# Performance work log

Measured on AMD Instinct MI355X. Metric: run time of the kernel, lower is better.

## Reference

```python
import jax, jax.numpy as jnp
import numpy as np

C = 64          # num_channels
DEPTH = 9       # dilation_depth
REPEAT = 2      # dilation_repeat
K = 2           # kernel_size
DILATIONS = [2 ** j for _ in range(REPEAT) for j in range(DEPTH)]
L = len(DILATIONS)  # 18 gated layers


def causal_conv(x, w, b, dilation):
    # x: [B, Cin, T], w: [Cout, Cin, K] -> [B, Cout, T] with causal (left) padding
    pad = (w.shape[-1] - 1) * dilation
    y = jax.lax.conv_general_dilated(
        x, w, window_strides=(1,), padding=[(pad, 0)],
        rhs_dilation=(dilation,), dimension_numbers=("NCH", "OIH", "NCH"))
    return y + b[None, :, None]


def setup_inputs() -> dict:
    key = jax.random.key(0)
    ks = jax.random.split(key, 9)
    s = 0.1
    x = jax.random.normal(ks[0], (4, 1, 65536), dtype=jnp.float32)
    in_w = jax.random.normal(ks[1], (C, 1, 1), dtype=jnp.float32) * s
    in_b = jax.random.normal(ks[2], (C,), dtype=jnp.float32) * s
    hid_w = jax.random.normal(ks[3], (L, 2 * C, C, K), dtype=jnp.float32) * s
    hid_b = jax.random.normal(ks[4], (L, 2 * C), dtype=jnp.float32) * s
    res_w = jax.random.normal(ks[5], (L, C, C, 1), dtype=jnp.float32) * s
    res_b = jax.random.normal(ks[6], (L, C), dtype=jnp.float32) * s
    mix_w = jax.random.normal(ks[7], (1, C * L, 1), dtype=jnp.float32) * s
    mix_b = jax.random.normal(ks[8], (1,), dtype=jnp.float32) * s
    return {"x": x, "in_w": in_w, "in_b": in_b, "hid_w": hid_w, "hid_b": hid_b,
            "res_w": res_w, "res_b": res_b, "mix_w": mix_w, "mix_b": mix_b}


def reference(x, in_w, in_b, hid_w, hid_b, res_w, res_b, mix_w, mix_b):
    # Input 1x1 conv: [B,1,T] -> [B,C,T]
    out = causal_conv(x, in_w, in_b, 1)
    skips = []
    for i, d in enumerate(DILATIONS):
        xi = out
        h = causal_conv(xi, hid_w[i], hid_b[i], d)       # [B, 2C, T]
        gated = jnp.tanh(h[:, :C]) * jax.nn.sigmoid(h[:, C:])  # [B, C, T]
        skips.append(gated)
        out = causal_conv(gated, res_w[i], res_b[i], 1) + xi    # residual
    skip = jnp.concatenate(skips, axis=1)                # [B, C*L, T]
    return causal_conv(skip, mix_w, mix_b, 1)            # [B, 1, T]
```

## Files before the change

kernel.cpp:

```cpp
#include <hip/hip_runtime.h>
#include <hip/hip_bf16.h>
#include <math.h>

#define NCH 64
#define T_LEN 65536
#define NLAYER 18

typedef __attribute__((ext_vector_type(8))) short bf16x8;
typedef __attribute__((ext_vector_type(4))) short bf16x4;
typedef __attribute__((ext_vector_type(4))) float f32x4;

static __device__ __forceinline__ float bf2f(short s) {
    union { short u[2]; float f; } v;
    v.u[0] = 0; v.u[1] = s;
    return v.f;
}

__global__ void input_conv_kernel(const float* __restrict__ x,
                                  const float* __restrict__ in_w,
                                  const float* __restrict__ in_b,
                                  __hip_bfloat16* __restrict__ out) {
    int gid = blockIdx.x * 256 + threadIdx.x;
    int c8 = gid & 7;
    int t  = (gid >> 3) & (T_LEN - 1);
    int b  = gid >> 19;
    float xv = x[(size_t)b * T_LEN + t];
    bf16x8 v;
#pragma unroll
    for (int j = 0; j < 8; ++j) {
        float o = in_w[c8 * 8 + j] * xv + in_b[c8 * 8 + j];
        __hip_bfloat16 h = __float2bfloat16(o);
        v[j] = *(short*)&h;
    }
    *(bf16x8*)(out + ((size_t)b * T_LEN + t) * NCH + c8 * 8) = v;
}

__global__ void convert_weights_kernel(const float* __restrict__ hid_w,
                                       const float* __restrict__ res_w,
                                       __hip_bfloat16* __restrict__ whid,
                                       __hip_bfloat16* __restrict__ wres) {
    int gid = blockIdx.x * 256 + threadIdx.x;
    if (gid < NLAYER * 128 * 128) {
        int l   = gid >> 14;
        int rem = gid & 16383;
        int o   = rem >> 7;
        int k   = rem & 127;
        float v = (k < 64)
            ? hid_w[((l * 128 + o) * 64 + k) * 2]
            : hid_w[((l * 128 + o) * 64 + (k - 64)) * 2 + 1];
        whid[gid] = __float2bfloat16(v);
    }
    if (gid < NLAYER * 64 * 64) {
        wres[gid] = __float2bfloat16(res_w[gid]);
    }
}

__global__ __launch_bounds__(256, 2) void layer_mfma_kernel(
    const __hip_bfloat16* __restrict__ prev,
    __hip_bfloat16* __restrict__ next,
    float* __restrict__ acc,
    const __hip_bfloat16* __restrict__ whid,
    const float* __restrict__ hb,
    const __hip_bfloat16* __restrict__ wres,
    const float* __restrict__ rb,
    const float* __restrict__ mw,
    int d) {
    __shared__ __align__(16) __hip_bfloat16 Xp[64 * 72];
    __shared__ __align__(16) __hip_bfloat16 Xc[64 * 72];
    __shared__ __align__(16) __hip_bfloat16 Gt[64 * 72];

    const int t0   = blockIdx.x << 6;
    const int tid  = threadIdx.x;
    const int lane = tid & 63;
    const int w4   = tid >> 6;
    const int l15  = lane & 15;
    const int quad = lane >> 4;
    const int m0   = w4 * 16;

    const int rr = tid >> 3;
    const int co = (tid & 7) * 8;

    bf16x8 aT[4], aS[4], aR[2];
    {
        const __hip_bfloat16* whT = whid + (size_t)(m0 + l15) * 128 + quad * 8;
        const __hip_bfloat16* whS = whT + 64 * 128;
#pragma unroll
        for (int k = 0; k < 4; ++k) {
            aT[k] = *(const bf16x8*)(whT + k * 32);
            aS[k] = *(const bf16x8*)(whS + k * 32);
        }
        const __hip_bfloat16* wrA = wres + (size_t)(m0 + l15) * 64 + quad * 8;
        aR[0] = *(const bf16x8*)(wrA);
        aR[1] = *(const bf16x8*)(wrA + 32);
    }
    f32x4 biasT, biasS, biasR;
#pragma unroll
    for (int r = 0; r < 4; ++r) {
        biasT[r] = hb[m0 + quad * 4 + r];
        biasS[r] = hb[64 + m0 + quad * 4 + r];
        biasR[r] = rb[m0 + quad * 4 + r];
    }
    float mwq[16];
#pragma unroll
    for (int j = 0; j < 16; ++j) mwq[j] = mw[quad * 16 + j];

    bf16x8 pc[2], pp[2];
#define LOAD_TILE(b)                                                          \
    do {                                                                      \
        const __hip_bfloat16* pb = prev + ((size_t)(b) * T_LEN + t0) * NCH;   \
        _Pragma("unroll")                                                     \
        for (int pass = 0; pass < 2; ++pass) {                                \
            int r = pass * 32 + rr;                                           \
            pc[pass] = *(const bf16x8*)(pb + r * NCH + co);                   \
            int tp = t0 + r - d;                                              \
            bf16x8 z = {0, 0, 0, 0, 0, 0, 0, 0};                              \
            pp[pass] = z;                                                     \
            if (tp >= 0)                                                      \
                pp[pass] = *(const bf16x8*)(prev +                            \
                    ((size_t)(b) * T_LEN + tp) * NCH + co);                   \
        }                                                                     \
    } while (0)

    LOAD_TILE(0);

#pragma unroll
    for (int b = 0; b < 4; ++b) {
#pragma unroll
        for (int pass = 0; pass < 2; ++pass) {
            int r = pass * 32 + rr;
            *(bf16x8*)(&Xc[r * 72 + co]) = pc[pass];
            *(bf16x8*)(&Xp[r * 72 + co]) = pp[pass];
        }
        __syncthreads();

        if (b < 3) LOAD_TILE(b + 1);

        f32x4 accT[4], accS[4];
#pragma unroll
        for (int nt = 0; nt < 4; ++nt) { accT[nt] = biasT; accS[nt] = biasS; }
#pragma unroll
        for (int ks = 0; ks < 4; ++ks) {
            const __hip_bfloat16* src = (ks < 2) ? Xp : Xc;
            const int kk = (ks & 1) * 32 + quad * 8;
#pragma unroll
            for (int nt = 0; nt < 4; ++nt) {
                bf16x8 bx = *(const bf16x8*)(&src[(nt * 16 + l15) * 72 + kk]);
                accT[nt] = __builtin_amdgcn_mfma_f32_16x16x32_bf16(aT[ks], bx, accT[nt], 0, 0, 0);
                accS[nt] = __builtin_amdgcn_mfma_f32_16x16x32_bf16(aS[ks], bx, accS[nt], 0, 0, 0);
            }
        }

#pragma unroll
        for (int nt = 0; nt < 4; ++nt) {
            int t = nt * 16 + l15;
#pragma unroll
            for (int r = 0; r < 4; ++r) {
                float e2 = __expf(2.f * accT[nt][r]);
                float th = 1.f - 2.f * __builtin_amdgcn_rcpf(e2 + 1.f);
                float sg = __builtin_amdgcn_rcpf(1.f + __expf(-accS[nt][r]));
                Gt[t * 72 + m0 + quad * 4 + r] = __float2bfloat16(th * sg);
            }
        }

        bf16x4 curres[4];
#pragma unroll
        for (int nt = 0; nt < 4; ++nt) {
            curres[nt] = *(const bf16x4*)(&Xc[(nt * 16 + l15) * 72 + m0 + quad * 4]);
        }
        __syncthreads();

        f32x4 accR[4];
#pragma unroll
        for (int nt = 0; nt < 4; ++nt) accR[nt] = biasR;
#pragma unroll
        for (int ks = 0; ks < 2; ++ks) {
            const int kk = ks * 32 + quad * 8;
#pragma unroll
            for (int nt = 0; nt < 4; ++nt) {
                bf16x8 bx = *(const bf16x8*)(&Gt[(nt * 16 + l15) * 72 + kk]);
                accR[nt] = __builtin_amdgcn_mfma_f32_16x16x32_bf16(aR[ks], bx, accR[nt], 0, 0, 0);
            }
        }

        __hip_bfloat16* nb = next + ((size_t)b * T_LEN + t0) * NCH;
#pragma unroll
        for (int nt = 0; nt < 4; ++nt) {
            int t = nt * 16 + l15;
            bf16x4 ov;
#pragma unroll
            for (int r = 0; r < 4; ++r) {
                __hip_bfloat16 h = __float2bfloat16(accR[nt][r] + bf2f(curres[nt][r]));
                ov[r] = *(short*)&h;
            }
            *(bf16x4*)(nb + t * NCH + m0 + quad * 4) = ov;
        }

        {
            int t = w4 * 16 + l15;
            bf16x8 g0 = *(const bf16x8*)(&Gt[t * 72 + quad * 16]);
            bf16x8 g1 = *(const bf16x8*)(&Gt[t * 72 + quad * 16 + 8]);
            float s = 0.f;
#pragma unroll
            for (int j = 0; j < 8; ++j) {
                s += mwq[j]     * bf2f(g0[j]);
                s += mwq[8 + j] * bf2f(g1[j]);
            }
            s += __shfl_xor(s, 16, 64);
            s += __shfl_xor(s, 32, 64);
            if (quad == 0)
                acc[(size_t)b * T_LEN + t0 + t] += s;
        }
    }
#undef LOAD_TILE
}

__global__ void finalize_kernel(const float* __restrict__ acc,
                                const float* __restrict__ mix_b,
                                float* __restrict__ out) {
    int gid = blockIdx.x * 256 + threadIdx.x;
    out[gid] = acc[gid] + mix_b[0];
}

extern "C" void kernel_launch(void* const* d_in, const int* in_sizes, int n_in,
                              void* d_out, int out_size, void* d_ws, size_t ws_size,
                              hipStream_t stream) {
    const float* x     = (const float*)d_in[0];
    const float* in_w  = (const float*)d_in[1];
    const float* in_b  = (const float*)d_in[2];
    const float* hid_w = (const float*)d_in[3];
    const float* hid_b = (const float*)d_in[4];
    const float* res_w = (const float*)d_in[5];
    const float* res_b = (const float*)d_in[6];
    const float* mix_w = (const float*)d_in[7];
    const float* mix_b = (const float*)d_in[8];
    float* out = (float*)d_out;

    const size_t act_elems = 4ull * T_LEN * NCH;
    __hip_bfloat16* actA = (__hip_bfloat16*)d_ws;
    __hip_bfloat16* actB = actA + act_elems;
    float* acc = (float*)(actB + act_elems);
    __hip_bfloat16* whid = (__hip_bfloat16*)(acc + 4ull * T_LEN);
    __hip_bfloat16* wres = whid + (size_t)NLAYER * 128 * 128;

    hipMemsetAsync(acc, 0, 4ull * T_LEN * sizeof(float), stream);

    convert_weights_kernel<<<1152, 256, 0, stream>>>(hid_w, res_w, whid, wres);

    input_conv_kernel<<<8192, 256, 0, stream>>>(x, in_w, in_b, actA);

    static const int dil[NLAYER] = {1, 2, 4, 8, 16, 32, 64, 128, 256,
                                    1, 2, 4, 8, 16, 32, 64, 128, 256};
    const __hip_bfloat16* cur = actA;
    __hip_bfloat16* nxt = actB;
    for (int i = 0; i < NLAYER; ++i) {
        layer_mfma_kernel<<<1024, 256, 0, stream>>>(
            cur, nxt, acc,
            whid + (size_t)i * 128 * 128,
            hid_b + (size_t)i * 128,
            wres + (size_t)i * 64 * 64,
            res_b + (size_t)i * 64,
            mix_w + (size_t)i * 64,
            dil[i]);
        const __hip_bfloat16* tmp = nxt;
        nxt = (__hip_bfloat16*)cur;
        cur = tmp;
    }

    finalize_kernel<<<1024, 256, 0, stream>>>(acc, mix_b, out);
}
```

Measured before the change: 592.9 us.

## Fuse six small-dilation layers per kernel with halo recompute and fold finalize into last layer

```diff
diff --git a/kernel.cpp b/kernel.cpp
--- a/kernel.cpp
+++ b/kernel.cpp
@@ -15,24 +15,9 @@
     v.u[0] = 0; v.u[1] = s;
     return v.f;
 }
-
-__global__ void input_conv_kernel(const float* __restrict__ x,
-                                  const float* __restrict__ in_w,
-                                  const float* __restrict__ in_b,
-                                  __hip_bfloat16* __restrict__ out) {
-    int gid = blockIdx.x * 256 + threadIdx.x;
-    int c8 = gid & 7;
-    int t  = (gid >> 3) & (T_LEN - 1);
-    int b  = gid >> 19;
-    float xv = x[(size_t)b * T_LEN + t];
-    bf16x8 v;
-#pragma unroll
-    for (int j = 0; j < 8; ++j) {
-        float o = in_w[c8 * 8 + j] * xv + in_b[c8 * 8 + j];
-        __hip_bfloat16 h = __float2bfloat16(o);
-        v[j] = *(short*)&h;
-    }
-    *(bf16x8*)(out + ((size_t)b * T_LEN + t) * NCH + c8 * 8) = v;
+static __device__ __forceinline__ short f2bf(float f) {
+    __hip_bfloat16 h = __float2bfloat16(f);
+    return *(short*)&h;
 }
 
 __global__ void convert_weights_kernel(const float* __restrict__ hid_w,
@@ -55,6 +40,203 @@
     }
 }
 
+__global__ __launch_bounds__(256, 2) void fused6_kernel(
+    const void* __restrict__ src,
+    __hip_bfloat16* __restrict__ next,
+    float* __restrict__ acc,
+    const __hip_bfloat16* __restrict__ whid_all,
+    const float* __restrict__ hb_all,
+    const __hip_bfloat16* __restrict__ wres_all,
+    const float* __restrict__ rb_all,
+    const float* __restrict__ mix_w,
+    const float* __restrict__ in_w,
+    const float* __restrict__ in_b,
+    int lbase, int is_first) {
+    __shared__ __align__(16) __hip_bfloat16 A[192 * 72];
+    __shared__ __align__(16) __hip_bfloat16 G[192 * 72];
+
+    const int b    = blockIdx.x >> 9;
+    const int widx = blockIdx.x & 511;
+    const int t0   = widx << 7;
+    const int tw   = t0 - 64;
+
+    const int tid  = threadIdx.x;
+    const int lane = tid & 63;
+    const int w4   = tid >> 6;
+    const int l15  = lane & 15;
+    const int quad = lane >> 4;
+    const int m0   = w4 * 16;
+    const int rr   = tid >> 3;
+    const int co   = (tid & 7) * 8;
+
+    if (is_first) {
+        const float* x = (const float*)src;
+        float iw[8], ib[8];
+#pragma unroll
+        for (int j = 0; j < 8; ++j) { iw[j] = in_w[co + j]; ib[j] = in_b[co + j]; }
+#pragma unroll
+        for (int round = 0; round < 6; ++round) {
+            int r  = round * 32 + rr;
+            int gt = tw + r;
+            bf16x8 v = {0, 0, 0, 0, 0, 0, 0, 0};
+            if (gt >= 0) {
+                float xv = x[(size_t)b * T_LEN + gt];
+#pragma unroll
+                for (int j = 0; j < 8; ++j) v[j] = f2bf(iw[j] * xv + ib[j]);
+            }
+            *(bf16x8*)(&A[r * 72 + co]) = v;
+        }
+    } else {
+        const __hip_bfloat16* prev = (const __hip_bfloat16*)src;
+#pragma unroll
+        for (int round = 0; round < 6; ++round) {
+            int r  = round * 32 + rr;
+            int gt = tw + r;
+            bf16x8 v = {0, 0, 0, 0, 0, 0, 0, 0};
+            if (gt >= 0)
+                v = *(const bf16x8*)(prev + ((size_t)b * T_LEN + gt) * NCH + co);
+            *(bf16x8*)(&A[r * 72 + co]) = v;
+        }
+    }
+
+    float skacc0 = 0.f, skacc1 = 0.f;
+
+#pragma unroll 1
+    for (int l = 0; l < 6; ++l) {
+        const int d = 1 << l;
+        const __hip_bfloat16* whid = whid_all + (size_t)(lbase + l) * 16384;
+        const __hip_bfloat16* wres = wres_all + (size_t)(lbase + l) * 4096;
+        const float* hb = hb_all + (lbase + l) * 128;
+        const float* rb = rb_all + (lbase + l) * 64;
+        const float* mw = mix_w + (lbase + l) * 64;
+
+        bf16x8 aT[4], aS[4], aR[2];
+        {
+            const __hip_bfloat16* whT = whid + (size_t)(m0 + l15) * 128 + quad * 8;
+            const __hip_bfloat16* whS = whT + 64 * 128;
+#pragma unroll
+            for (int k = 0; k < 4; ++k) {
+                aT[k] = *(const bf16x8*)(whT + k * 32);
+                aS[k] = *(const bf16x8*)(whS + k * 32);
+            }
+            const __hip_bfloat16* wrA = wres + (size_t)(m0 + l15) * 64 + quad * 8;
+            aR[0] = *(const bf16x8*)(wrA);
+            aR[1] = *(const bf16x8*)(wrA + 32);
+        }
+        f32x4 biasT, biasS, biasR;
+#pragma unroll
+        for (int r = 0; r < 4; ++r) {
+            biasT[r] = hb[m0 + quad * 4 + r];
+            biasS[r] = hb[64 + m0 + quad * 4 + r];
+            biasR[r] = rb[m0 + quad * 4 + r];
+        }
+        float mwq[16];
+#pragma unroll
+        for (int k = 0; k < 4; ++k) {
+            float4 m4 = *(const float4*)(mw + quad * 16 + k * 4);
+            mwq[k * 4 + 0] = m4.x; mwq[k * 4 + 1] = m4.y;
+            mwq[k * 4 + 2] = m4.z; mwq[k * 4 + 3] = m4.w;
+        }
+
+        __syncthreads();
+
+#pragma unroll
+        for (int ct = 0; ct < 3; ++ct) {
+            f32x4 accT[4], accS[4];
+#pragma unroll
+            for (int nt = 0; nt < 4; ++nt) { accT[nt] = biasT; accS[nt] = biasS; }
+#pragma unroll
+            for (int ks = 0; ks < 4; ++ks) {
+                const int koff = (ks & 1) * 32 + quad * 8;
+#pragma unroll
+                for (int nt = 0; nt < 4; ++nt) {
+                    int trow = ct * 64 + nt * 16 + l15;
+                    int prow = trow - d;  prow = prow < 0 ? 0 : prow;
+                    int row  = (ks < 2) ? prow : trow;
+                    bf16x8 bx = *(const bf16x8*)(&A[row * 72 + koff]);
+                    accT[nt] = __builtin_amdgcn_mfma_f32_16x16x32_bf16(aT[ks], bx, accT[nt], 0, 0, 0);
+                    accS[nt] = __builtin_amdgcn_mfma_f32_16x16x32_bf16(aS[ks], bx, accS[nt], 0, 0, 0);
+                }
+            }
+#pragma unroll
+            for (int nt = 0; nt < 4; ++nt) {
+                int trow = ct * 64 + nt * 16 + l15;
+                bf16x4 gv;
+#pragma unroll
+                for (int r = 0; r < 4; ++r) {
+                    float e2 = __expf(2.f * accT[nt][r]);
+                    float th = 1.f - 2.f * __builtin_amdgcn_rcpf(e2 + 1.f);
+                    float sg = __builtin_amdgcn_rcpf(1.f + __expf(-accS[nt][r]));
+                    gv[r] = f2bf(th * sg);
+                }
+                *(bf16x4*)(&G[trow * 72 + m0 + quad * 4]) = gv;
+            }
+        }
+        __syncthreads();
+
+#pragma unroll
+        for (int ct = 0; ct < 3; ++ct) {
+            f32x4 accR[4];
+#pragma unroll
+            for (int nt = 0; nt < 4; ++nt) accR[nt] = biasR;
+#pragma unroll
+            for (int ks = 0; ks < 2; ++ks) {
+                const int koff = ks * 32 + quad * 8;
+#pragma unroll
+                for (int nt = 0; nt < 4; ++nt) {
+                    int trow = ct * 64 + nt * 16 + l15;
+                    bf16x8 bx = *(const bf16x8*)(&G[trow * 72 + koff]);
+                    accR[nt] = __builtin_amdgcn_mfma_f32_16x16x32_bf16(aR[ks], bx, accR[nt], 0, 0, 0);
+                }
+            }
+#pragma unroll
+            for (int nt = 0; nt < 4; ++nt) {
+                int trow = ct * 64 + nt * 16 + l15;
+                bf16x4 old = *(const bf16x4*)(&A[trow * 72 + m0 + quad * 4]);
+                bool ok = (tw + trow) >= 0;
+                bf16x4 ov;
+#pragma unroll
+                for (int r = 0; r < 4; ++r) {
+                    float v = accR[nt][r] + bf2f(old[r]);
+                    ov[r] = f2bf(ok ? v : 0.f);
+                }
+                *(bf16x4*)(&A[trow * 72 + m0 + quad * 4]) = ov;
+            }
+        }
+
+#pragma unroll
+        for (int s = 0; s < 2; ++s) {
+            int p = 64 + w4 * 32 + s * 16 + l15;
+            bf16x8 g0 = *(const bf16x8*)(&G[p * 72 + quad * 16]);
+            bf16x8 g1 = *(const bf16x8*)(&G[p * 72 + quad * 16 + 8]);
+            float sv = 0.f;
+#pragma unroll
+            for (int j = 0; j < 8; ++j) {
+                sv += mwq[j]     * bf2f(g0[j]);
+                sv += mwq[8 + j] * bf2f(g1[j]);
+            }
+            if (s == 0) skacc0 += sv; else skacc1 += sv;
+        }
+    }
+    __syncthreads();
+
+#pragma unroll
+    for (int round = 0; round < 4; ++round) {
+        int pr = round * 32 + rr;
+        *(bf16x8*)(next + ((size_t)b * T_LEN + t0 + pr) * NCH + co) =
+            *(const bf16x8*)(&A[(pr + 64) * 72 + co]);
+    }
+
+    skacc0 += __shfl_xor(skacc0, 16, 64);
+    skacc0 += __shfl_xor(skacc0, 32, 64);
+    skacc1 += __shfl_xor(skacc1, 16, 64);
+    skacc1 += __shfl_xor(skacc1, 32, 64);
+    if (quad == 0) {
+        acc[(size_t)b * T_LEN + t0 + w4 * 32 + l15]      += skacc0;
+        acc[(size_t)b * T_LEN + t0 + w4 * 32 + 16 + l15] += skacc1;
+    }
+}
+
 __global__ __launch_bounds__(256, 2) void layer_mfma_kernel(
     const __hip_bfloat16* __restrict__ prev,
     __hip_bfloat16* __restrict__ next,
@@ -76,7 +258,6 @@
     const int l15  = lane & 15;
     const int quad = lane >> 4;
     const int m0   = w4 * 16;
-
     const int rr = tid >> 3;
     const int co = (tid & 7) * 8;
 
@@ -140,11 +321,11 @@
         for (int nt = 0; nt < 4; ++nt) { accT[nt] = biasT; accS[nt] = biasS; }
 #pragma unroll
         for (int ks = 0; ks < 4; ++ks) {
-            const __hip_bfloat16* src = (ks < 2) ? Xp : Xc;
+            const __hip_bfloat16* srcb = (ks < 2) ? Xp : Xc;
             const int kk = (ks & 1) * 32 + quad * 8;
 #pragma unroll
             for (int nt = 0; nt < 4; ++nt) {
-                bf16x8 bx = *(const bf16x8*)(&src[(nt * 16 + l15) * 72 + kk]);
+                bf16x8 bx = *(const bf16x8*)(&srcb[(nt * 16 + l15) * 72 + kk]);
                 accT[nt] = __builtin_amdgcn_mfma_f32_16x16x32_bf16(aT[ks], bx, accT[nt], 0, 0, 0);
                 accS[nt] = __builtin_amdgcn_mfma_f32_16x16x32_bf16(aS[ks], bx, accS[nt], 0, 0, 0);
             }
@@ -189,8 +370,7 @@
             bf16x4 ov;
 #pragma unroll
             for (int r = 0; r < 4; ++r) {
-                __hip_bfloat16 h = __float2bfloat16(accR[nt][r] + bf2f(curres[nt][r]));
-                ov[r] = *(short*)&h;
+                ov[r] = f2bf(accR[nt][r] + bf2f(curres[nt][r]));
             }
             *(bf16x4*)(nb + t * NCH + m0 + quad * 4) = ov;
         }
@@ -214,11 +394,119 @@
 #undef LOAD_TILE
 }
 
-__global__ void finalize_kernel(const float* __restrict__ acc,
-                                const float* __restrict__ mix_b,
-                                float* __restrict__ out) {
-    int gid = blockIdx.x * 256 + threadIdx.x;
-    out[gid] = acc[gid] + mix_b[0];
+__global__ __launch_bounds__(256, 2) void last_layer_kernel(
+    const __hip_bfloat16* __restrict__ prev,
+    const float* __restrict__ acc,
+    float* __restrict__ out,
+    const __hip_bfloat16* __restrict__ whid,
+    const float* __restrict__ hb,
+    const float* __restrict__ mw,
+    const float* __restrict__ mix_b,
+    int d) {
+    __shared__ __align__(16) __hip_bfloat16 Xp[64 * 72];
+    __shared__ __align__(16) __hip_bfloat16 Xc[64 * 72];
+    __shared__ float skb[4 * 64];
+
+    const int t0   = blockIdx.x << 6;
+    const int tid  = threadIdx.x;
+    const int lane = tid & 63;
+    const int w4   = tid >> 6;
+    const int l15  = lane & 15;
+    const int quad = lane >> 4;
+    const int m0   = w4 * 16;
+    const int rr = tid >> 3;
+    const int co = (tid & 7) * 8;
+
+    bf16x8 aT[4], aS[4];
+    {
+        const __hip_bfloat16* whT = whid + (size_t)(m0 + l15) * 128 + quad * 8;
+        const __hip_bfloat16* whS = whT + 64 * 128;
+#pragma unroll
+        for (int k = 0; k < 4; ++k) {
+            aT[k] = *(const bf16x8*)(whT + k * 32);
+            aS[k] = *(const bf16x8*)(whS + k * 32);
+        }
+    }
+    f32x4 biasT, biasS;
+    float mwv[4];
+#pragma unroll
+    for (int r = 0; r < 4; ++r) {
+        biasT[r] = hb[m0 + quad * 4 + r];
+        biasS[r] = hb[64 + m0 + quad * 4 + r];
+        mwv[r]   = mw[m0 + quad * 4 + r];
+    }
+    const float mb = mix_b[0];
+
+    bf16x8 pc[2], pp[2];
+#define LOAD_TILE(b)                                                          \
+    do {                                                                      \
+        const __hip_bfloat16* pb = prev + ((size_t)(b) * T_LEN + t0) * NCH;   \
+        _Pragma("unroll")                                                     \
+        for (int pass = 0; pass < 2; ++pass) {                                \
+            int r = pass * 32 + rr;                                           \
+            pc[pass] = *(const bf16x8*)(pb + r * NCH + co);                   \
+            int tp = t0 + r - d;                                              \
+            bf16x8 z = {0, 0, 0, 0, 0, 0, 0, 0};                              \
+            pp[pass] = z;                                                     \
+            if (tp >= 0)                                                      \
+                pp[pass] = *(const bf16x8*)(prev +                            \
+                    ((size_t)(b) * T_LEN + tp) * NCH + co);                   \
+        }                                                                     \
+    } while (0)
+
+    LOAD_TILE(0);
+
+#pragma unroll
+    for (int b = 0; b < 4; ++b) {
+#pragma unroll
+        for (int pass = 0; pass < 2; ++pass) {
+            int r = pass * 32 + rr;
+            *(bf16x8*)(&Xc[r * 72 + co]) = pc[pass];
+            *(bf16x8*)(&Xp[r * 72 + co]) = pp[pass];
+        }
+        __syncthreads();
+
+        if (b < 3) LOAD_TILE(b + 1);
+
+        f32x4 accT[4], accS[4];
+#pragma unroll
+        for (int nt = 0; nt < 4; ++nt) { accT[nt] = biasT; accS[nt] = biasS; }
+#pragma unroll
+        for (int ks = 0; ks < 4; ++ks) {
+            const __hip_bfloat16* srcb = (ks < 2) ? Xp : Xc;
+            const int kk = (ks & 1) * 32 + quad * 8;
+#pragma unroll
+            for (int nt = 0; nt < 4; ++nt) {
+                bf16x8 bx = *(const bf16x8*)(&srcb[(nt * 16 + l15) * 72 + kk]);
+                accT[nt] = __builtin_amdgcn_mfma_f32_16x16x32_bf16(aT[ks], bx, accT[nt], 0, 0, 0);
+                accS[nt] = __builtin_amdgcn_mfma_f32_16x16x32_bf16(aS[ks], bx, accS[nt], 0, 0, 0);
+            }
+        }
+
+#pragma unroll
+        for (int nt = 0; nt < 4; ++nt) {
+            float sv = 0.f;
+#pragma unroll
+            for (int r = 0; r < 4; ++r) {
+                float e2 = __expf(2.f * accT[nt][r]);
+                float th = 1.f - 2.f * __builtin_amdgcn_rcpf(e2 + 1.f);
+                float sg = __builtin_amdgcn_rcpf(1.f + __expf(-accS[nt][r]));
+                sv += mwv[r] * (th * sg);
+            }
+            sv += __shfl_xor(sv, 16, 64);
+            sv += __shfl_xor(sv, 32, 64);
+            if (quad == 0)
+                skb[w4 * 64 + nt * 16 + l15] = sv;
+        }
+        __syncthreads();
+
+        if (tid < 64) {
+            float tot = skb[tid] + skb[64 + tid] + skb[128 + tid] + skb[192 + tid];
+            out[(size_t)b * T_LEN + t0 + tid] =
+                acc[(size_t)b * T_LEN + t0 + tid] + tot + mb;
+        }
+    }
+#undef LOAD_TILE
 }
 
 extern "C" void kernel_launch(void* const* d_in, const int* in_sizes, int n_in,
@@ -246,25 +534,30 @@
 
     convert_weights_kernel<<<1152, 256, 0, stream>>>(hid_w, res_w, whid, wres);
 
-    input_conv_kernel<<<8192, 256, 0, stream>>>(x, in_w, in_b, actA);
-
-    static const int dil[NLAYER] = {1, 2, 4, 8, 16, 32, 64, 128, 256,
-                                    1, 2, 4, 8, 16, 32, 64, 128, 256};
-    const __hip_bfloat16* cur = actA;
-    __hip_bfloat16* nxt = actB;
-    for (int i = 0; i < NLAYER; ++i) {
-        layer_mfma_kernel<<<1024, 256, 0, stream>>>(
-            cur, nxt, acc,
-            whid + (size_t)i * 128 * 128,
-            hid_b + (size_t)i * 128,
-            wres + (size_t)i * 64 * 64,
-            res_b + (size_t)i * 64,
-            mix_w + (size_t)i * 64,
-            dil[i]);
-        const __hip_bfloat16* tmp = nxt;
-        nxt = (__hip_bfloat16*)cur;
-        cur = tmp;
-    }
-
-    finalize_kernel<<<1024, 256, 0, stream>>>(acc, mix_b, out);
-}
+    fused6_kernel<<<2048, 256, 0, stream>>>(
+        x, actA, acc, whid, hid_b, wres, res_b, mix_w, in_w, in_b, 0, 1);
+
+    layer_mfma_kernel<<<1024, 256, 0, stream>>>(
+        actA, actB, acc, whid + 6 * 16384, hid_b + 6 * 128,
+        wres + 6 * 4096, res_b + 6 * 64, mix_w + 6 * 64, 64);
+    layer_mfma_kernel<<<1024, 256, 0, stream>>>(
+        actB, actA, acc, whid + 7 * 16384, hid_b + 7 * 128,
+        wres + 7 * 4096, res_b + 7 * 64, mix_w + 7 * 64, 128);
+    layer_mfma_kernel<<<1024, 256, 0, stream>>>(
+        actA, actB, acc, whid + 8 * 16384, hid_b + 8 * 128,
+        wres + 8 * 4096, res_b + 8 * 64, mix_w + 8 * 64, 256);
+
+    fused6_kernel<<<2048, 256, 0, stream>>>(
+        actB, actA, acc, whid, hid_b, wres, res_b, mix_w, in_w, in_b, 9, 0);
+
+    layer_mfma_kernel<<<1024, 256, 0, stream>>>(
+        actA, actB, acc, whid + 15 * 16384, hid_b + 15 * 128,
+        wres + 15 * 4096, res_b + 15 * 64, mix_w + 15 * 64, 64);
+    layer_mfma_kernel<<<1024, 256, 0, stream>>>(
+        actB, actA, acc, whid + 16 * 16384, hid_b + 16 * 128,
+        wres + 16 * 4096, res_b + 16 * 64, mix_w + 16 * 64, 128);
+
+    last_layer_kernel<<<1024, 256, 0, stream>>>(
+        actA, acc, out, whid + 17 * 16384, hid_b + 17 * 128,
+        mix_w + 17 * 64, mix_b, 256);
+}
```

After: 556.0 us. 1.07x faster.
